# Optimization experiments

Measured on AMD Instinct MI355X. Metric: run time of the kernel, lower is better.

Reference implementation:

```python
import jax, jax.numpy as jnp
import numpy as np

B, N = 4, 8192
NPOINT, NSAMPLE = 2048, 16
IN_PLANES, OUT_PLANES = 64, 128
EPS = 1e-5


def farthest_point_sample(xyz, npoint):
    # xyz: (B, N, 3) -> (B, npoint) int32 indices. Deterministic start at index 0
    # (torch version uses a random start; fixed start keeps the reference reproducible).
    Bb, Nn, _ = xyz.shape

    def step(carry, _):
        distance, farthest = carry                                   # (B,N), (B,)
        centroid = jnp.take_along_axis(xyz, farthest[:, None, None], axis=1)  # (B,1,3)
        dist = jnp.sum((xyz - centroid) ** 2, axis=-1)               # (B,N)
        distance = jnp.minimum(distance, dist)
        new_farthest = jnp.argmax(distance, axis=-1).astype(jnp.int32)
        return (distance, new_farthest), farthest

    init = (jnp.full((Bb, Nn), 1e10, xyz.dtype), jnp.zeros((Bb,), jnp.int32))
    _, cents = jax.lax.scan(step, init, None, length=npoint)         # (npoint, B)
    return cents.T                                                   # (B, npoint)


def setup_inputs() -> dict:
    key = jax.random.key(0)
    k1, k2, k3 = jax.random.split(key, 3)
    px = jax.random.normal(k1, (B, N, IN_PLANES), jnp.float32)
    xyz = jax.random.uniform(k2, (B, N, 3), jnp.float32)
    # Linear(3+in_planes -> out_planes), stored as (in, out)
    W = jax.random.normal(k3, (3 + IN_PLANES, OUT_PLANES), jnp.float32) * 0.1
    b = jnp.zeros((OUT_PLANES,), jnp.float32)
    gamma = jnp.ones((OUT_PLANES,), jnp.float32)
    beta = jnp.zeros((OUT_PLANES,), jnp.float32)
    return {"px": px, "xyz": xyz, "W": W, "b": b, "gamma": gamma, "beta": beta}


def reference(px, xyz, W, b, gamma, beta):
    Bb, Nn, C = px.shape
    cent_idx = farthest_point_sample(xyz, NPOINT)                    # (B, npoint)
    new_xyz = jnp.take_along_axis(xyz, cent_idx[:, :, None], axis=1) # (B, npoint, 3)

    # squared pairwise distances, clamped at 0 (matches square_distance)
    dists = (jnp.sum(new_xyz ** 2, -1)[..., None]
             + jnp.sum(xyz ** 2, -1)[:, None, :]
             - 2.0 * jnp.einsum('bmc,bnc->bmn', new_xyz, xyz))       # (B, npoint, N)
    dists = jnp.maximum(dists, 0.0)

    # KNN: top_k on negated dists == argsort()[:, :, :nsample] up to ties
    _, idx = jax.lax.top_k(-dists, NSAMPLE)                          # (B, npoint, nsample)

    gather = jax.vmap(lambda pts, i: pts[i])                         # per-batch fancy gather
    grouped_xyz = gather(xyz, idx)                                   # (B, npoint, nsample, 3)
    grouped_px = gather(px, idx)                                     # (B, npoint, nsample, C)
    grouped_xyz_norm = grouped_xyz - new_xyz[:, :, None, :]
    grouped = jnp.concatenate([grouped_px, grouped_xyz_norm], axis=-1)

    # Linear -> BatchNorm1d (training-mode batch stats, biased var) -> ReLU
    h = grouped.reshape(-1, C + 3) @ W + b                           # (B*npoint*nsample, out)
    mu = jnp.mean(h, axis=0)
    var = jnp.var(h, axis=0)
    h = (h - mu) / jnp.sqrt(var + EPS) * gamma + beta
    h = jax.nn.relu(h)

    new_px = jnp.max(h.reshape(Bb, NPOINT, NSAMPLE, -1), axis=2)     # (B, npoint, out)
    return new_px, new_xyz
```

## Files before the change

kernel.cpp:

```cpp
#include <hip/hip_runtime.h>
#include <math.h>

#define Bc 4
#define Nc 8192
#define NPOINTc 2048
#define NSAMPLEc 16
#define CINc 64
#define COUTc 128
#define FDIMc 67
#define NBUCK 128
#define EPSc 1e-5f

typedef unsigned long long u64;

__global__ void sq_norm_kernel(const float* __restrict__ xyz, float* __restrict__ sn) {
    int i = blockIdx.x * blockDim.x + threadIdx.x;
    if (i < Bc * Nc) {
        float x = xyz[i * 3], y = xyz[i * 3 + 1], z = xyz[i * 3 + 2];
        sn[i] = __fadd_rn(__fadd_rn(__fmul_rn(x, x), __fmul_rn(y, y)), __fmul_rn(z, z));
    }
}

template <int CTRL>
__device__ __forceinline__ float dpp_maxf(float x) {
    const float o = __int_as_float(__builtin_amdgcn_update_dpp(
        __float_as_int(x), __float_as_int(x), CTRL, 0xF, 0xF, false));
    return fmaxf(x, o);
}
template <int CTRL>
__device__ __forceinline__ float dpp_minf(float x) {
    const float o = __int_as_float(__builtin_amdgcn_update_dpp(
        __float_as_int(x), __float_as_int(x), CTRL, 0xF, 0xF, false));
    return fminf(x, o);
}
template <int CTRL>
__device__ __forceinline__ unsigned dpp_minu(unsigned x) {
    const unsigned o = (unsigned)__builtin_amdgcn_update_dpp((int)x, (int)x, CTRL, 0xF, 0xF, false);
    return (o < x) ? o : x;
}
template <int CTRL>
__device__ __forceinline__ void kmax_dpp(u64& key) {
    const unsigned lo = (unsigned)key, hi = (unsigned)(key >> 32);
    const unsigned olo = (unsigned)__builtin_amdgcn_update_dpp((int)lo, (int)lo, CTRL, 0xF, 0xF, false);
    const unsigned ohi = (unsigned)__builtin_amdgcn_update_dpp((int)hi, (int)hi, CTRL, 0xF, 0xF, false);
    const u64 okey = ((u64)ohi << 32) | olo;
    key = (okey > key) ? okey : key;
}

__global__ __launch_bounds__(512) void fps_kernel(const float* __restrict__ xyz,
                                                  int* __restrict__ cent,
                                                  float* __restrict__ newxyz) {
    const int b = blockIdx.x;
    const float* base = xyz + (size_t)b * Nc * 3;
    const int t = threadIdx.x;
    const int lane = t & 63, wid = t >> 6;

    __shared__ float P[Nc * 3];
    __shared__ u64   pk[2][8];
    __shared__ int   WIN[NPOINTc];

    for (int e = t; e < Nc * 3; e += 512) P[e] = base[e];

    float X[16], Y[16], Z[16], D[16];
#pragma unroll
    for (int k = 0; k < 16; ++k) {
        const int n = t + (k << 9);
        X[k] = base[n * 3 + 0];
        Y[k] = base[n * 3 + 1];
        Z[k] = base[n * 3 + 2];
        D[k] = 1e10f;
    }
    if (t == 0) WIN[0] = 0;
    __syncthreads();

    float cx = P[0], cy = P[1], cz = P[2];

    for (int it = 1; it < NPOINTc; ++it) {
#pragma unroll
        for (int k = 0; k < 16; ++k) {
            const float dx = __fsub_rn(X[k], cx);
            const float dy = __fsub_rn(Y[k], cy);
            const float dz = __fsub_rn(Z[k], cz);
            const float d2 = __fadd_rn(__fadd_rn(__fmul_rn(dx, dx), __fmul_rn(dy, dy)),
                                       __fmul_rn(dz, dz));
            D[k] = fminf(D[k], d2);
        }
        float a0[8]; int x0[8];
#pragma unroll
        for (int k = 0; k < 8; ++k) {
            const bool g = D[2 * k + 1] > D[2 * k];
            a0[k] = g ? D[2 * k + 1] : D[2 * k];
            x0[k] = t + ((g ? (2 * k + 1) : (2 * k)) << 9);
        }
        float a1[4]; int x1[4];
#pragma unroll
        for (int k = 0; k < 4; ++k) {
            const bool g = a0[2 * k + 1] > a0[2 * k];
            a1[k] = g ? a0[2 * k + 1] : a0[2 * k];
            x1[k] = g ? x0[2 * k + 1] : x0[2 * k];
        }
        float a2[2]; int x2[2];
#pragma unroll
        for (int k = 0; k < 2; ++k) {
            const bool g = a1[2 * k + 1] > a1[2 * k];
            a2[k] = g ? a1[2 * k + 1] : a1[2 * k];
            x2[k] = g ? x1[2 * k + 1] : x1[2 * k];
        }
        const bool gf = a2[1] > a2[0];
        const float bd = gf ? a2[1] : a2[0];
        const int   bi = gf ? x2[1] : x2[0];

        float wv = bd;
        wv = dpp_maxf<0x111>(wv);
        wv = dpp_maxf<0x112>(wv);
        wv = dpp_maxf<0x114>(wv);
        wv = dpp_maxf<0x118>(wv);
        wv = dpp_maxf<0x142>(wv);
        wv = dpp_maxf<0x143>(wv);
        const float v = __int_as_float(__builtin_amdgcn_readlane(__float_as_int(wv), 63));

        unsigned cand = (bd == v) ? (unsigned)bi : 0xffffffffu;
        cand = dpp_minu<0x111>(cand);
        cand = dpp_minu<0x112>(cand);
        cand = dpp_minu<0x114>(cand);
        cand = dpp_minu<0x118>(cand);
        cand = dpp_minu<0x142>(cand);
        cand = dpp_minu<0x143>(cand);

        const int par = it & 1;
        if (lane == 63) pk[par][wid] = ((u64)__float_as_uint(v) << 32) | (unsigned)(~cand);
        __syncthreads();

        u64 k8 = pk[par][lane & 7];
        if (lane >= 8) k8 = 0;
        kmax_dpp<0x111>(k8);
        kmax_dpp<0x112>(k8);
        kmax_dpp<0x114>(k8);
        const unsigned lo7 = (unsigned)__builtin_amdgcn_readlane((int)(unsigned)k8, 7);
        const int riv = (int)~lo7;

        cx = P[riv * 3 + 0]; cy = P[riv * 3 + 1]; cz = P[riv * 3 + 2];
        if (t == 0) WIN[it] = riv;
    }
    __syncthreads();

    for (int e = t; e < NPOINTc; e += 512) {
        const int wv2 = WIN[e];
        cent[b * NPOINTc + e] = wv2;
        float* o = newxyz + ((size_t)b * NPOINTc + e) * 3;
        o[0] = P[wv2 * 3 + 0]; o[1] = P[wv2 * 3 + 1]; o[2] = P[wv2 * 3 + 2];
    }
}

__global__ __launch_bounds__(64) void knn_kernel(const float* __restrict__ xyz,
                                                 const float* __restrict__ sn,
                                                 const int* __restrict__ cent,
                                                 int* __restrict__ knn) {
    const int g = blockIdx.x;
    const int b = g >> 11;
    const int lane = threadIdx.x;
    const float* base = xyz + (size_t)b * Nc * 3;
    const float* snb = sn + (size_t)b * Nc;

    const int cm = cent[g];
    const float mx = base[cm * 3 + 0];
    const float my = base[cm * 3 + 1];
    const float mz = base[cm * 3 + 2];
    const float s1 = snb[cm];

    float dls[16];
    int   ils[16];
#pragma unroll
    for (int j = 0; j < 16; ++j) { dls[j] = INFINITY; ils[j] = -1; }

    for (int jj = 0; jj < Nc / 64; ++jj) {
        const int n = lane + (jj << 6);
        const float x = base[n * 3 + 0];
        const float y = base[n * 3 + 1];
        const float z = base[n * 3 + 2];
        const float dot = fmaf(z, mz, fmaf(y, my, __fmul_rn(x, mx)));
        float d = __fadd_rn(__fadd_rn(__fmul_rn(-2.0f, dot), s1), snb[n]);
        d = fmaxf(d, 0.0f);
        if (d < dls[15]) {
            float cd = d; int ci = n;
#pragma unroll
            for (int j = 0; j < 16; ++j) {
                const bool less = cd < dls[j];
                const float td = less ? dls[j] : cd;
                const int   ti = less ? ils[j] : ci;
                dls[j] = less ? cd : dls[j];
                ils[j] = less ? ci : ils[j];
                cd = td; ci = ti;
            }
        }
    }

    __shared__ float ld[64][17];
    __shared__ int   li[64][17];
#pragma unroll
    for (int j = 0; j < 16; ++j) { ld[lane][j] = dls[j]; li[lane][j] = ils[j]; }

    int ptr = 0;
    int res = 0;
    int* out = knn + (size_t)g * NSAMPLEc;
    for (int r = 0; r < NSAMPLEc; ++r) {
        const float hd = ld[lane][ptr];
        const int   hi = li[lane][ptr];

        float vd = hd;
        vd = dpp_minf<0x111>(vd);
        vd = dpp_minf<0x112>(vd);
        vd = dpp_minf<0x114>(vd);
        vd = dpp_minf<0x118>(vd);
        vd = dpp_minf<0x142>(vd);
        vd = dpp_minf<0x143>(vd);
        const float v = __int_as_float(__builtin_amdgcn_readlane(__float_as_int(vd), 63));

        unsigned cand = (hd == v) ? (unsigned)hi : 0xffffffffu;
        cand = dpp_minu<0x111>(cand);
        cand = dpp_minu<0x112>(cand);
        cand = dpp_minu<0x114>(cand);
        cand = dpp_minu<0x118>(cand);
        cand = dpp_minu<0x142>(cand);
        cand = dpp_minu<0x143>(cand);
        const int win = (int)(unsigned)__builtin_amdgcn_readlane((int)cand, 63);

        if (hd == v && hi == win) ptr++;
        if (lane == r) res = win;
    }
    if (lane < NSAMPLEc) out[lane] = res;
}

__device__ __forceinline__ void stage_featT(
        const float* __restrict__ px, const float* __restrict__ xyz,
        const float* __restrict__ newxyz, const int* __restrict__ knn,
        int g, int b, int t, float (*featT)[20], int* nidx, float* ctr) {
    if (t < 16) nidx[t] = knn[(size_t)g * NSAMPLEc + t];
    if (t < 3)  ctr[t] = newxyz[(size_t)g * 3 + t];
    __syncthreads();
    for (int e = t; e < 16 * FDIMc; e += 128) {
        const int s = e / FDIMc, i = e % FDIMc;
        float v;
        if (i < CINc) v = px[((size_t)b * Nc + nidx[s]) * CINc + i];
        else          v = __fsub_rn(xyz[((size_t)b * Nc + nidx[s]) * 3 + (i - CINc)], ctr[i - CINc]);
        featT[i][s] = v;
    }
    __syncthreads();
}

__device__ __forceinline__ void gemm_body(const float (*featT)[20], const float* __restrict__ W,
                                          float bc, int t, float* acc) {
#pragma unroll
    for (int r = 0; r < 16; ++r) acc[r] = bc;
    for (int i = 0; i < FDIMc; ++i) {
        const float w = W[i * COUTc + t];
        const float4* fr = (const float4*)featT[i];
        const float4 f0 = fr[0], f1 = fr[1], f2 = fr[2], f3 = fr[3];
        acc[0]  = fmaf(f0.x, w, acc[0]);  acc[1]  = fmaf(f0.y, w, acc[1]);
        acc[2]  = fmaf(f0.z, w, acc[2]);  acc[3]  = fmaf(f0.w, w, acc[3]);
        acc[4]  = fmaf(f1.x, w, acc[4]);  acc[5]  = fmaf(f1.y, w, acc[5]);
        acc[6]  = fmaf(f1.z, w, acc[6]);  acc[7]  = fmaf(f1.w, w, acc[7]);
        acc[8]  = fmaf(f2.x, w, acc[8]);  acc[9]  = fmaf(f2.y, w, acc[9]);
        acc[10] = fmaf(f2.z, w, acc[10]); acc[11] = fmaf(f2.w, w, acc[11]);
        acc[12] = fmaf(f3.x, w, acc[12]); acc[13] = fmaf(f3.y, w, acc[13]);
        acc[14] = fmaf(f3.z, w, acc[14]); acc[15] = fmaf(f3.w, w, acc[15]);
    }
}

__global__ __launch_bounds__(128) void gemm_stats_kernel(
        const float* __restrict__ px, const float* __restrict__ xyz,
        const float* __restrict__ newxyz, const int* __restrict__ knn,
        const float* __restrict__ W, const float* __restrict__ bias,
        float* __restrict__ bsum, float* __restrict__ bsq,
        float* __restrict__ hmax_out) {
    const int g = blockIdx.x;
    const int b = g >> 11;
    const int t = threadIdx.x;

    __shared__ __align__(16) float featT[FDIMc][20];
    __shared__ int nidx[16];
    __shared__ float ctr[3];
    stage_featT(px, xyz, newxyz, knn, g, b, t, featT, nidx, ctr);

    float acc[16];
    gemm_body(featT, W, bias[t], t, acc);

    float s = 0.f, q = 0.f, mx = acc[0];
#pragma unroll
    for (int r = 0; r < 16; ++r) { s += acc[r]; q += acc[r] * acc[r]; }
#pragma unroll
    for (int r = 1; r < 16; ++r) mx = fmaxf(mx, acc[r]);
    atomicAdd(&bsum[(g & (NBUCK - 1)) * COUTc + t], s);
    atomicAdd(&bsq [(g & (NBUCK - 1)) * COUTc + t], q);
    hmax_out[(size_t)g * COUTc + t] = mx;
}

__global__ __launch_bounds__(128) void stats_finalize_kernel(
        const float* __restrict__ bsum, const float* __restrict__ bsq,
        const float* __restrict__ gamma, const float* __restrict__ beta,
        float* __restrict__ scsh) {
    const int c = blockIdx.x;
    const int k = threadIdx.x;
    __shared__ float sS[128], sQ[128];
    sS[k] = bsum[k * COUTc + c];
    sQ[k] = bsq[k * COUTc + c];
    __syncthreads();
    for (int s = 64; s > 0; s >>= 1) {
        if (k < s) { sS[k] += sS[k + s]; sQ[k] += sQ[k + s]; }
        __syncthreads();
    }
    if (k == 0) {
        const float cnt = (float)(Bc * NPOINTc * NSAMPLEc);
        const float mu = sS[0] / cnt;
        const float var = sQ[0] / cnt - mu * mu;
        const float sc = gamma[c] / sqrtf(var + EPSc);
        scsh[c] = sc;
        scsh[COUTc + c] = beta[c] - mu * sc;
        if (!(sc > 0.f)) atomicAdd(&scsh[2 * COUTc], 1.0f);
    }
}

__global__ __launch_bounds__(256) void finalize_out_kernel(
        const float* __restrict__ scsh, float* __restrict__ out) {
    const int i = blockIdx.x * 256 + threadIdx.x;
    const int c = i & (COUTc - 1);
    const float sc = scsh[c], sh = scsh[COUTc + c];
    out[i] = fmaxf(fmaf(out[i], sc, sh), 0.0f);
}

__global__ __launch_bounds__(128) void guard_negsc_kernel(
        const float* __restrict__ px, const float* __restrict__ xyz,
        const float* __restrict__ newxyz, const int* __restrict__ knn,
        const float* __restrict__ W, const float* __restrict__ bias,
        const float* __restrict__ scsh, float* __restrict__ out) {
    if (scsh[2 * COUTc] == 0.0f) return;
    const int g = blockIdx.x;
    const int b = g >> 11;
    const int t = threadIdx.x;

    __shared__ __align__(16) float featT[FDIMc][20];
    __shared__ int nidx[16];
    __shared__ float ctr[3];
    stage_featT(px, xyz, newxyz, knn, g, b, t, featT, nidx, ctr);

    float acc[16];
    gemm_body(featT, W, bias[t], t, acc);

    const float sc = scsh[t], sh = scsh[COUTc + t];
    if (sc > 0.f) return;
    float m = -INFINITY;
#pragma unroll
    for (int r = 0; r < 16; ++r) m = fmaxf(m, fmaxf(fmaf(acc[r], sc, sh), 0.0f));
    out[(size_t)g * COUTc + t] = m;
}

extern "C" void kernel_launch(void* const* d_in, const int* in_sizes, int n_in,
                              void* d_out, int out_size, void* d_ws, size_t ws_size,
                              hipStream_t stream) {
    const float* px    = (const float*)d_in[0];
    const float* xyz   = (const float*)d_in[1];
    const float* W     = (const float*)d_in[2];
    const float* bias  = (const float*)d_in[3];
    const float* gamma = (const float*)d_in[4];
    const float* beta  = (const float*)d_in[5];

    float* out_px = (float*)d_out;
    float* out_nx = out_px + (size_t)Bc * NPOINTc * COUTc;

    char* w = (char*)d_ws;
    int*   cent = (int*)w;    w += (size_t)Bc * NPOINTc * 4;
    float* sn   = (float*)w;  w += (size_t)Bc * Nc * 4;
    int*   knn  = (int*)w;    w += (size_t)Bc * NPOINTc * NSAMPLEc * 4;
    float* bsum = (float*)w;  w += (size_t)NBUCK * COUTc * 4;
    float* bsq  = (float*)w;  w += (size_t)NBUCK * COUTc * 4;
    float* scsh = (float*)w;  w += (2 * COUTc + 4) * 4;

    hipMemsetAsync(bsum, 0, (size_t)NBUCK * COUTc * 4 * 2 + (2 * COUTc + 4) * 4, stream);

    sq_norm_kernel<<<(Bc * Nc + 255) / 256, 256, 0, stream>>>(xyz, sn);
    fps_kernel<<<Bc, 512, 0, stream>>>(xyz, cent, out_nx);
    knn_kernel<<<Bc * NPOINTc, 64, 0, stream>>>(xyz, sn, cent, knn);
    gemm_stats_kernel<<<Bc * NPOINTc, 128, 0, stream>>>(px, xyz, out_nx, knn, W, bias,
                                                        bsum, bsq, out_px);
    stats_finalize_kernel<<<COUTc, 128, 0, stream>>>(bsum, bsq, gamma, beta, scsh);
    finalize_out_kernel<<<(Bc * NPOINTc * COUTc) / 256, 256, 0, stream>>>(scsh, out_px);
    guard_negsc_kernel<<<Bc * NPOINTc, 128, 0, stream>>>(px, xyz, out_nx, knn, W, bias, scsh, out_px);
}
```

Measured before the change: 2.697 ms.

## Sort FPS points by Morton code and skip waves via bounding-box bound

Before the FPS loop, points are bucketed by a 12-bit Morton code using a shared-memory histogram and scan. Each wave then owns a spatially coherent chunk and computes its bounding box. In each iteration a wave skips its distance update and reduction when the box lower bound cannot beat its previous max, reusing the cached key. This removes per-iteration distance work for far-away clusters, at the cost of a sorting prologue, more shared memory, and index tie-breaking that must still match argmax order.

```diff
diff --git a/kernel.cpp b/kernel.cpp
--- a/kernel.cpp
+++ b/kernel.cpp
@@ -46,6 +46,16 @@
     const u64 okey = ((u64)ohi << 32) | olo;
     key = (okey > key) ? okey : key;
 }
+__device__ __forceinline__ float wave_minf(float x) {
+    x = dpp_minf<0x111>(x); x = dpp_minf<0x112>(x); x = dpp_minf<0x114>(x);
+    x = dpp_minf<0x118>(x); x = dpp_minf<0x142>(x); x = dpp_minf<0x143>(x);
+    return __int_as_float(__builtin_amdgcn_readlane(__float_as_int(x), 63));
+}
+__device__ __forceinline__ float wave_maxf(float x) {
+    x = dpp_maxf<0x111>(x); x = dpp_maxf<0x112>(x); x = dpp_maxf<0x114>(x);
+    x = dpp_maxf<0x118>(x); x = dpp_maxf<0x142>(x); x = dpp_maxf<0x143>(x);
+    return __int_as_float(__builtin_amdgcn_readlane(__float_as_int(x), 63));
+}
 
 __global__ __launch_bounds__(512) void fps_kernel(const float* __restrict__ xyz,
                                                   int* __restrict__ cent,
@@ -58,77 +68,137 @@
     __shared__ float P[Nc * 3];
     __shared__ u64   pk[2][8];
     __shared__ int   WIN[NPOINTc];
+    __shared__ int   hist[4096];
+    __shared__ int   sidx[Nc];
+    __shared__ int   scanb[512];
 
     for (int e = t; e < Nc * 3; e += 512) P[e] = base[e];
-
-    float X[16], Y[16], Z[16], D[16];
-#pragma unroll
-    for (int k = 0; k < 16; ++k) {
-        const int n = t + (k << 9);
-        X[k] = base[n * 3 + 0];
-        Y[k] = base[n * 3 + 1];
-        Z[k] = base[n * 3 + 2];
-        D[k] = 1e10f;
-    }
+    for (int e = t; e < 4096; e += 512) hist[e] = 0;
+    __syncthreads();
+
+    unsigned mc[16];
+#pragma unroll
+    for (int j = 0; j < 16; ++j) {
+        const int n = t * 16 + j;
+        const float x = P[n * 3], y = P[n * 3 + 1], z = P[n * 3 + 2];
+        const unsigned xi = (unsigned)fminf(fmaxf(x * 16.f, 0.f), 15.f);
+        const unsigned yi = (unsigned)fminf(fmaxf(y * 16.f, 0.f), 15.f);
+        const unsigned zi = (unsigned)fminf(fmaxf(z * 16.f, 0.f), 15.f);
+        unsigned c = 0;
+#pragma unroll
+        for (int bb = 0; bb < 4; ++bb)
+            c |= (((xi >> bb) & 1u) << (3 * bb + 2)) | (((yi >> bb) & 1u) << (3 * bb + 1))
+               | (((zi >> bb) & 1u) << (3 * bb));
+        mc[j] = c;
+        atomicAdd(&hist[c], 1);
+    }
+    __syncthreads();
+
+    int loc[8]; int s = 0;
+#pragma unroll
+    for (int j = 0; j < 8; ++j) { loc[j] = s; s += hist[t * 8 + j]; }
+    scanb[t] = s;
+    __syncthreads();
+    for (int off = 1; off < 512; off <<= 1) {
+        const int add = (t >= off) ? scanb[t - off] : 0;
+        __syncthreads();
+        scanb[t] += add;
+        __syncthreads();
+    }
+    const int base_off = scanb[t] - s;
+#pragma unroll
+    for (int j = 0; j < 8; ++j) hist[t * 8 + j] = base_off + loc[j];
+    __syncthreads();
+
+#pragma unroll
+    for (int j = 0; j < 16; ++j) {
+        const int slot = atomicAdd(&hist[mc[j]], 1);
+        sidx[slot] = t * 16 + j;
+    }
+    __syncthreads();
+
+    const int ms = (wid & 4) ? (wid ^ 3) : wid;
+    float X[16], Y[16], Z[16], D[16]; int I[16];
+    float bx0 = 1e30f, bx1 = -1e30f, by0 = 1e30f, by1 = -1e30f, bz0 = 1e30f, bz1 = -1e30f;
+#pragma unroll
+    for (int j = 0; j < 16; ++j) {
+        const int si = sidx[ms * 1024 + lane * 16 + j];
+        I[j] = si;
+        const float x = P[si * 3], y = P[si * 3 + 1], z = P[si * 3 + 2];
+        X[j] = x; Y[j] = y; Z[j] = z; D[j] = 1e10f;
+        bx0 = fminf(bx0, x); bx1 = fmaxf(bx1, x);
+        by0 = fminf(by0, y); by1 = fmaxf(by1, y);
+        bz0 = fminf(bz0, z); bz1 = fmaxf(bz1, z);
+    }
+    const float wbx0 = wave_minf(bx0), wbx1 = wave_maxf(bx1);
+    const float wby0 = wave_minf(by0), wby1 = wave_maxf(by1);
+    const float wbz0 = wave_minf(bz0), wbz1 = wave_maxf(bz1);
+
     if (t == 0) WIN[0] = 0;
     __syncthreads();
 
     float cx = P[0], cy = P[1], cz = P[2];
+    float vprev = 1e30f;
+    u64 kw = 0;
 
     for (int it = 1; it < NPOINTc; ++it) {
-#pragma unroll
-        for (int k = 0; k < 16; ++k) {
-            const float dx = __fsub_rn(X[k], cx);
-            const float dy = __fsub_rn(Y[k], cy);
-            const float dz = __fsub_rn(Z[k], cz);
-            const float d2 = __fadd_rn(__fadd_rn(__fmul_rn(dx, dx), __fmul_rn(dy, dy)),
-                                       __fmul_rn(dz, dz));
-            D[k] = fminf(D[k], d2);
+        const float gx = fmaxf(0.f, fmaxf(wbx0 - cx, cx - wbx1));
+        const float gy = fmaxf(0.f, fmaxf(wby0 - cy, cy - wby1));
+        const float gz = fmaxf(0.f, fmaxf(wbz0 - cz, cz - wbz1));
+        const float lb = (gx * gx + gy * gy) + gz * gz;
+        if (__fmul_rn(lb, 0.99999f) < vprev) {
+#pragma unroll
+            for (int k = 0; k < 16; ++k) {
+                const float dx = __fsub_rn(X[k], cx);
+                const float dy = __fsub_rn(Y[k], cy);
+                const float dz = __fsub_rn(Z[k], cz);
+                const float d2 = __fadd_rn(__fadd_rn(__fmul_rn(dx, dx), __fmul_rn(dy, dy)),
+                                           __fmul_rn(dz, dz));
+                D[k] = fminf(D[k], d2);
+            }
+            float td0[8]; int ti0[8];
+#pragma unroll
+            for (int k = 0; k < 8; ++k) {
+                const bool g = (D[2 * k + 1] > D[2 * k]) ||
+                               (D[2 * k + 1] == D[2 * k] && I[2 * k + 1] < I[2 * k]);
+                td0[k] = g ? D[2 * k + 1] : D[2 * k];
+                ti0[k] = g ? I[2 * k + 1] : I[2 * k];
+            }
+            float td1[4]; int ti1[4];
+#pragma unroll
+            for (int k = 0; k < 4; ++k) {
+                const bool g = (td1[0], (td0[2 * k + 1] > td0[2 * k]) ||
+                               (td0[2 * k + 1] == td0[2 * k] && ti0[2 * k + 1] < ti0[2 * k]));
+                td1[k] = g ? td0[2 * k + 1] : td0[2 * k];
+                ti1[k] = g ? ti0[2 * k + 1] : ti0[2 * k];
+            }
+            float td2[2]; int ti2[2];
+#pragma unroll
+            for (int k = 0; k < 2; ++k) {
+                const bool g = (td1[2 * k + 1] > td1[2 * k]) ||
+                               (td1[2 * k + 1] == td1[2 * k] && ti1[2 * k + 1] < ti1[2 * k]);
+                td2[k] = g ? td1[2 * k + 1] : td1[2 * k];
+                ti2[k] = g ? ti1[2 * k + 1] : ti1[2 * k];
+            }
+            const bool gf = (td2[1] > td2[0]) || (td2[1] == td2[0] && ti2[1] < ti2[0]);
+            const float bd = gf ? td2[1] : td2[0];
+            const int   bi = gf ? ti2[1] : ti2[0];
+
+            const float v = wave_maxf(bd);
+            unsigned cand = (bd == v) ? (unsigned)bi : 0xffffffffu;
+            cand = dpp_minu<0x111>(cand);
+            cand = dpp_minu<0x112>(cand);
+            cand = dpp_minu<0x114>(cand);
+            cand = dpp_minu<0x118>(cand);
+            cand = dpp_minu<0x142>(cand);
+            cand = dpp_minu<0x143>(cand);
+            const unsigned candw = (unsigned)__builtin_amdgcn_readlane((int)cand, 63);
+
+            vprev = v;
+            kw = ((u64)__float_as_uint(v) << 32) | (unsigned)(~candw);
         }
-        float a0[8]; int x0[8];
-#pragma unroll
-        for (int k = 0; k < 8; ++k) {
-            const bool g = D[2 * k + 1] > D[2 * k];
-            a0[k] = g ? D[2 * k + 1] : D[2 * k];
-            x0[k] = t + ((g ? (2 * k + 1) : (2 * k)) << 9);
-        }
-        float a1[4]; int x1[4];
-#pragma unroll
-        for (int k = 0; k < 4; ++k) {
-            const bool g = a0[2 * k + 1] > a0[2 * k];
-            a1[k] = g ? a0[2 * k + 1] : a0[2 * k];
-            x1[k] = g ? x0[2 * k + 1] : x0[2 * k];
-        }
-        float a2[2]; int x2[2];
-#pragma unroll
-        for (int k = 0; k < 2; ++k) {
-            const bool g = a1[2 * k + 1] > a1[2 * k];
-            a2[k] = g ? a1[2 * k + 1] : a1[2 * k];
-            x2[k] = g ? x1[2 * k + 1] : x1[2 * k];
-        }
-        const bool gf = a2[1] > a2[0];
-        const float bd = gf ? a2[1] : a2[0];
-        const int   bi = gf ? x2[1] : x2[0];
-
-        float wv = bd;
-        wv = dpp_maxf<0x111>(wv);
-        wv = dpp_maxf<0x112>(wv);
-        wv = dpp_maxf<0x114>(wv);
-        wv = dpp_maxf<0x118>(wv);
-        wv = dpp_maxf<0x142>(wv);
-        wv = dpp_maxf<0x143>(wv);
-        const float v = __int_as_float(__builtin_amdgcn_readlane(__float_as_int(wv), 63));
-
-        unsigned cand = (bd == v) ? (unsigned)bi : 0xffffffffu;
-        cand = dpp_minu<0x111>(cand);
-        cand = dpp_minu<0x112>(cand);
-        cand = dpp_minu<0x114>(cand);
-        cand = dpp_minu<0x118>(cand);
-        cand = dpp_minu<0x142>(cand);
-        cand = dpp_minu<0x143>(cand);
-
         const int par = it & 1;
-        if (lane == 63) pk[par][wid] = ((u64)__float_as_uint(v) << 32) | (unsigned)(~cand);
+        if (lane == 63) pk[par][wid] = kw;
         __syncthreads();
 
         u64 k8 = pk[par][lane & 7];
```

Result: slower. 5.001 ms (+85.4%).
